# Optimization experiments

Hardware: AMD Instinct MI355X
Metric: run time of the kernel (lower is better)

## Reference

```python
import jax, jax.numpy as jnp
import numpy as np

N = 100000      # num_nodes
E = 1600000     # num_edges
IN_DIM = 6
EDGE_DIM = 2
H = 5           # heads
C = 5           # out_channels per head (hidden_dim)
D = H * C       # 25, hidden width
L = 3           # num_layers
INV_SQRT_C = np.float32(1.0 / np.sqrt(C))


def setup_inputs() -> dict:
    key = jax.random.key(0)
    ks = jax.random.split(key, 18)
    s = 0.1
    inp = {
        "x": jax.random.normal(ks[0], (N, IN_DIM), dtype=jnp.float32),
        "edge_index": jax.random.randint(ks[1], (2, E), 0, N, dtype=jnp.int64),
        "edge_attr": jax.random.normal(ks[2], (E, EDGE_DIM), dtype=jnp.float32),
        # input projection
        "Wi": jax.random.normal(ks[3], (IN_DIM, D), dtype=jnp.float32) * s,
        "bi": jnp.zeros((D,), dtype=jnp.float32),
        # per-layer TransformerConv params, stacked over layers
        "Wq": jax.random.normal(ks[4], (L, D, D), dtype=jnp.float32) * s,
        "bq": jnp.zeros((L, D), dtype=jnp.float32),
        "Wk": jax.random.normal(ks[5], (L, D, D), dtype=jnp.float32) * s,
        "bk": jnp.zeros((L, D), dtype=jnp.float32),
        "Wv": jax.random.normal(ks[6], (L, D, D), dtype=jnp.float32) * s,
        "bv": jnp.zeros((L, D), dtype=jnp.float32),
        "We": jax.random.normal(ks[7], (L, EDGE_DIM, D), dtype=jnp.float32) * s,  # lin_edge, no bias
        "Wskip": jax.random.normal(ks[8], (L, D, D), dtype=jnp.float32) * s,
        "bskip": jnp.zeros((L, D), dtype=jnp.float32),
        # output head
        "Wo": jax.random.normal(ks[9], (D, 1), dtype=jnp.float32) * s,
        "bo": jnp.zeros((1,), dtype=jnp.float32),
    }
    return inp


def _forward(x, edge_index, edge_attr, Wi, bi, Wq, bq, Wk, bk, Wv, bv, We, Wskip, bskip, Wo, bo):
    src, dst = edge_index[0], edge_index[1]
    h = x @ Wi + bi  # [N, D]
    for l in range(L):
        q = (h @ Wq[l] + bq[l]).reshape(N, H, C)
        k = (h @ Wk[l] + bk[l]).reshape(N, H, C)
        v = (h @ Wv[l] + bv[l]).reshape(N, H, C)
        e = (edge_attr @ We[l]).reshape(E, H, C)  # per-edge projection
        k_j = k[src] + e                           # [E, H, C]
        alpha = jnp.einsum('ehc,ehc->eh', q[dst], k_j) * INV_SQRT_C  # [E, H]
        # scatter-softmax over destination neighborhoods (PyG softmax)
        amax = jax.ops.segment_max(alpha, dst, num_segments=N)       # [N, H]
        ex = jnp.exp(alpha - amax[dst])
        denom = jax.ops.segment_sum(ex, dst, num_segments=N)         # [N, H]
        alpha = ex / (denom[dst] + 1e-16)
        msg = (v[src] + e) * alpha[:, :, None]                       # [E, H, C]
        out = jax.ops.segment_sum(msg, dst, num_segments=N).reshape(N, D)
        h = out + h @ Wskip[l] + bskip[l]          # root_weight skip
    return jax.nn.sigmoid(h @ Wo + bo)             # [N, 1]


def reference(x, edge_index, edge_attr, Wi, bi, Wq, bq, Wk, bk, Wv, bv, We, Wskip, bskip, Wo, bo):
    return _forward(x, edge_index, edge_attr, Wi, bi, Wq, bq, Wk, bk, Wv, bv, We, Wskip, bskip, Wo, bo)
```

## Files before the change

### kernel.cpp

```cpp
#include <hip/hip_runtime.h>
#include <hip/hip_bf16.h>
#include <math.h>

#define NN 100000
#define NE 1600000
#define IN_DIM 6
#define EDGE_DIM 2
#define HH 5
#define CC 5
#define DD 25
#define DS 32
#define INV_SQRT_C 0.4472135954999579f
#define NBUK 200
#define BUKW 500
#define CAP 10000
#define KPB 800
#define CH (NE / KPB)
#define NPB 48
#define NBLK ((NN + NPB - 1) / NPB)
#define NBD ((NN + 255) / 256)


__device__ __forceinline__ unsigned int f2bf(float f) {
    unsigned int u = __float_as_uint(f);
    return (u + 0x7fffu + ((u >> 16) & 1u)) >> 16;
}
__device__ __forceinline__ float bflo(unsigned int u) { return __uint_as_float(u << 16); }
__device__ __forceinline__ float bfhi(unsigned int u) { return __uint_as_float(u & 0xffff0000u); }

__global__ __launch_bounds__(256) void k_part(const int* __restrict__ ei,
                                              const float* __restrict__ ea,
                                              int* __restrict__ cursor,
                                              uint2* __restrict__ slab) {
    __shared__ int sdst[CH];
    __shared__ int scnt[NBUK];
    __shared__ int sbase[NBUK];
    __shared__ int swp[NBUK];
    int base = blockIdx.x * CH;
    for (int i = threadIdx.x; i < NBUK; i += 256) scnt[i] = 0;
    __syncthreads();
    for (int i = threadIdx.x; i < CH; i += 256) {
        int dst = ei[NE + base + i];
        sdst[i] = dst;
        atomicAdd(&scnt[dst / BUKW], 1);
    }
    __syncthreads();
    for (int i = threadIdx.x; i < NBUK; i += 256) {
        sbase[i] = i * CAP + atomicAdd(&cursor[i], scnt[i]);
        swp[i] = 0;
    }
    __syncthreads();
    for (int i = threadIdx.x; i < CH; i += 256) {
        int dst = sdst[i];
        int b = dst / BUKW;
        int src = ei[base + i];
        float2 eav = ((const float2*)ea)[base + i];
        int p = sbase[b] + atomicAdd(&swp[b], 1);
        uint2 r;
        r.x = (unsigned)src | ((unsigned)(dst - b * BUKW) << 17);
        r.y = f2bf(eav.x) | (f2bf(eav.y) << 16);
        slab[p] = r;
    }
}

__global__ __launch_bounds__(512) void k_place(const int* __restrict__ cursor,
                                               const uint2* __restrict__ slab,
                                               int* __restrict__ rowptr,
                                               uint2* __restrict__ csr) {
    __shared__ int hist[BUKW];
    __shared__ int cur[BUKW];
    __shared__ int s[512];
    int b = blockIdx.x;
    int t = threadIdx.x;
    int node0 = b * BUKW;
    int begin = b * CAP;
    int cnt = cursor[b];
    s[t] = (t < NBUK && t < b) ? cursor[t] : 0;
    __syncthreads();
    for (int off = 256; off > 0; off >>= 1) {
        if (t < off) s[t] += s[t + off];
        __syncthreads();
    }
    int bOff = s[0];
    __syncthreads();
    for (int i = t; i < BUKW; i += 512) hist[i] = 0;
    __syncthreads();
    for (int i = t; i < cnt; i += 512) {
        uint2 r = slab[begin + i];
        atomicAdd(&hist[r.x >> 17], 1);
    }
    __syncthreads();
    int hv = (t < BUKW) ? hist[t] : 0;
    s[t] = hv;
    __syncthreads();
    for (int off = 1; off < 512; off <<= 1) {
        int u = (t >= off) ? s[t - off] : 0;
        __syncthreads();
        s[t] += u;
        __syncthreads();
    }
    if (t < BUKW) {
        int o = bOff + s[t] - hv;
        rowptr[node0 + t] = o;
        cur[t] = o;
    }
    if (b == NBUK - 1 && t == 0) rowptr[NN] = NE;
    __syncthreads();
    for (int i = t; i < cnt; i += 512) {
        uint2 r = slab[begin + i];
        int dl = (int)(r.x >> 17);
        int p = atomicAdd(&cur[dl], 1);
        uint2 o;
        o.x = r.x & 0x1FFFFu;
        o.y = r.y;
        csr[p] = o;
    }
}

__global__ void k_dh(const int* __restrict__ rowptr, int* __restrict__ bhist) {
    __shared__ int lh[256];
    int t = threadIdx.x;
    lh[t] = 0;
    __syncthreads();
    int i = blockIdx.x * 256 + t;
    if (i < NN) {
        int d = rowptr[i + 1] - rowptr[i];
        atomicAdd(&lh[d > 255 ? 255 : d], 1);
    }
    __syncthreads();
    bhist[t * NBD + blockIdx.x] = lh[t];
}

__global__ __launch_bounds__(512) void k_ds(int* __restrict__ bhist, int* __restrict__ binTot) {
    __shared__ int s[512];
    int bin = blockIdx.x;
    int t = threadIdx.x;
    int v = (t < NBD) ? bhist[bin * NBD + t] : 0;
    s[t] = v;
    __syncthreads();
    for (int off = 1; off < 512; off <<= 1) {
        int u = (t >= off) ? s[t - off] : 0;
        __syncthreads();
        s[t] += u;
        __syncthreads();
    }
    if (t < NBD) bhist[bin * NBD + t] = s[t] - v;
    if (t == 511) binTot[bin] = s[511];
}

__global__ void k_ds2(int* __restrict__ binTot, int* __restrict__ binOff) {
    __shared__ int s[256];
    int t = threadIdx.x;
    int v = binTot[t];
    s[t] = v;
    __syncthreads();
    for (int off = 1; off < 256; off <<= 1) {
        int u = (t >= off) ? s[t - off] : 0;
        __syncthreads();
        s[t] += u;
        __syncthreads();
    }
    binOff[t] = s[t] - v;
}

__global__ void k_dp(const int* __restrict__ rowptr, const int* __restrict__ bhist,
                     const int* __restrict__ binOff, int* __restrict__ perm) {
    __shared__ int lcur[256];
    int t = threadIdx.x;
    lcur[t] = 0;
    __syncthreads();
    int i = blockIdx.x * 256 + t;
    if (i < NN) {
        int d = rowptr[i + 1] - rowptr[i];
        if (d > 255) d = 255;
        int r = atomicAdd(&lcur[d], 1);
        perm[binOff[d] + bhist[d * NBD + blockIdx.x] + r] = i;
    }
}

__global__ void k_input_proj(const float* __restrict__ x, const float* __restrict__ Wi,
                             const float* __restrict__ bi, float* __restrict__ h) {
    __shared__ float sW[IN_DIM * DD];
    __shared__ float sb[DD];
    int t = threadIdx.x;
    if (t < IN_DIM * DD) sW[t] = Wi[t];
    if (t < DD) sb[t] = bi[t];
    __syncthreads();
    int tid = blockIdx.x * blockDim.x + t;
    int n = tid / DD, d = tid - n * DD;
    if (n >= NN) return;
    float acc = sb[d];
    const float* xr = x + n * IN_DIM;
#pragma unroll
    for (int i = 0; i < IN_DIM; i++) acc += xr[i] * sW[i * DD + d];
    h[n * DS + d] = acc;
}

__global__ void k_qkv_skip(const float* __restrict__ h,
                           const float* __restrict__ Wq, const float* __restrict__ bq,
                           const float* __restrict__ Wk, const float* __restrict__ bk,
                           const float* __restrict__ Wv, const float* __restrict__ bv,
                           const float* __restrict__ Ws, const float* __restrict__ bs,
                           __hip_bfloat16* __restrict__ q, __hip_bfloat16* __restrict__ kv,
                           float* __restrict__ hout) {
    __shared__ float sWq[DD * DD], sWk[DD * DD], sWv[DD * DD], sWs[DD * DD];
    __shared__ float sb[4 * DD];
    for (int i = threadIdx.x; i < DD * DD; i += blockDim.x) {
        sWq[i] = Wq[i]; sWk[i] = Wk[i]; sWv[i] = Wv[i]; sWs[i] = Ws[i];
    }
    if (threadIdx.x < DD) {
        sb[threadIdx.x]          = bq[threadIdx.x];
        sb[DD + threadIdx.x]     = bk[threadIdx.x];
        sb[2 * DD + threadIdx.x] = bv[threadIdx.x];
        sb[3 * DD + threadIdx.x] = bs[threadIdx.x];
    }
    __syncthreads();
    int tid = blockIdx.x * blockDim.x + threadIdx.x;
    int n = tid / DD, d = tid - n * DD;
    if (n >= NN) return;
    float aq = sb[d], ak = sb[DD + d], av = sb[2 * DD + d], asv = sb[3 * DD + d];
    const float* hr = h + (size_t)n * DS;
#pragma unroll
    for (int i = 0; i < DD; i++) {
        float hv = hr[i];
        aq  += hv * sWq[i * DD + d];
        ak  += hv * sWk[i * DD + d];
        av  += hv * sWv[i * DD + d];
        asv += hv * sWs[i * DD + d];
    }
    int h5 = d / 5, c5 = d - 5 * h5;
    q[(size_t)n * 40 + 8 * h5 + c5] = __float2bfloat16(aq * INV_SQRT_C);
    size_t rb = (size_t)n * 64;
    kv[rb + 8 * h5 + c5] = __float2bfloat16(ak);
    if (c5 < 3) kv[rb + 8 * h5 + 5 + c5] = __float2bfloat16(av);
    else        kv[rb + 40 + 2 * h5 + (c5 - 3)] = __float2bfloat16(av);
    hout[(size_t)n * DS + d] = asv;
}

__global__ __launch_bounds__(256) void k_edge_fused(
    const int* __restrict__ rowptr, const uint2* __restrict__ csr,
    const int* __restrict__ perm,
    const float* __restrict__ We, const __hip_bfloat16* __restrict__ q,
    const __hip_bfloat16* __restrict__ kv, float* __restrict__ hout,
    int fuse_head, const float* __restrict__ Wo, const float* __restrict__ bo,
    float* __restrict__ out) {
    __shared__ float sWe[EDGE_DIM * DD];
    __shared__ float sWo[DD];
    __shared__ float sbo;
    if (threadIdx.x < EDGE_DIM * DD) sWe[threadIdx.x] = We[threadIdx.x];
    if (threadIdx.x < DD) sWo[threadIdx.x] = Wo[threadIdx.x];
    if (threadIdx.x == 0) sbo = bo[0];
    __syncthreads();
    int lane = threadIdx.x & 63;
    int wv   = threadIdx.x >> 6;
    int grp  = lane / 5;
    int h    = lane - grp * 5;
    int idx  = blockIdx.x * NPB + wv * 12 + grp;
    bool act = (grp < 12) && (idx < NN);
    int node = 0;

    int beg = 0, end = 0;
    float qa0 = 0, qa1 = 0, qa2 = 0, qa3 = 0, qa4 = 0, qwx = 0, qwy = 0;
    if (act) {
        node = perm[idx];
        beg = rowptr[node];
        end = rowptr[node + 1];
        uint4 qc = *(const uint4*)(q + (size_t)node * 40 + 8 * h);
        qa0 = bflo(qc.x); qa1 = bfhi(qc.x); qa2 = bflo(qc.y); qa3 = bfhi(qc.y); qa4 = bflo(qc.z);
        const float* wx = &sWe[5 * h];
        const float* wy = &sWe[DD + 5 * h];
        qwx = qa0 * wx[0] + qa1 * wx[1] + qa2 * wx[2] + qa3 * wx[3] + qa4 * wx[4];
        qwy = qa0 * wy[0] + qa1 * wy[1] + qa2 * wy[2] + qa3 * wy[3] + qa4 * wy[4];
    }

    float l = 0.f, Sx = 0.f, Sy = 0.f;
    float a0 = 0.f, a1 = 0.f, a2 = 0.f, a3 = 0.f, a4 = 0.f;

    int p = beg;
    for (; p + 2 <= end; p += 2) {
        uint2 r0 = csr[p];
        uint2 r1 = csr[p + 1];
        const __hip_bfloat16* b0 = kv + ((size_t)r0.x << 6);
        const __hip_bfloat16* b1 = kv + ((size_t)r1.x << 6);
        uint4 A0 = *(const uint4*)(b0 + 8 * h);
        unsigned int B0 = *(const unsigned int*)(b0 + 40 + 2 * h);
        uint4 A1 = *(const uint4*)(b1 + 8 * h);
        unsigned int B1 = *(const unsigned int*)(b1 + 40 + 2 * h);
        {
            float eax = bflo(r0.y), eay = bfhi(r0.y);
            float k0 = bflo(A0.x), k1 = bfhi(A0.x), k2 = bflo(A0.y), k3 = bfhi(A0.y), k4 = bflo(A0.z);
            float v0 = bfhi(A0.z), v1 = bflo(A0.w), v2 = bfhi(A0.w), v3 = bflo(B0), v4 = bfhi(B0);
            float s = qa0 * k0 + qa1 * k1 + qa2 * k2 + qa3 * k3 + qa4 * k4 + eax * qwx + eay * qwy;
            float cf = __expf(s);
            l += cf; Sx += cf * eax; Sy += cf * eay;
            a0 += cf * v0; a1 += cf * v1; a2 += cf * v2; a3 += cf * v3; a4 += cf * v4;
        }
        {
            float eax = bflo(r1.y), eay = bfhi(r1.y);
            float k0 = bflo(A1.x), k1 = bfhi(A1.x), k2 = bflo(A1.y), k3 = bfhi(A1.y), k4 = bflo(A1.z);
            float v0 = bfhi(A1.z), v1 = bflo(A1.w), v2 = bfhi(A1.w), v3 = bflo(B1), v4 = bfhi(B1);
            float s = qa0 * k0 + qa1 * k1 + qa2 * k2 + qa3 * k3 + qa4 * k4 + eax * qwx + eay * qwy;
            float cf = __expf(s);
            l += cf; Sx += cf * eax; Sy += cf * eay;
            a0 += cf * v0; a1 += cf * v1; a2 += cf * v2; a3 += cf * v3; a4 += cf * v4;
        }
    }
    if (p < end) {
        uint2 r0 = csr[p];
        const __hip_bfloat16* b0 = kv + ((size_t)r0.x << 6);
        uint4 A0 = *(const uint4*)(b0 + 8 * h);
        unsigned int B0 = *(const unsigned int*)(b0 + 40 + 2 * h);
        float eax = bflo(r0.y), eay = bfhi(r0.y);
        float k0 = bflo(A0.x), k1 = bfhi(A0.x), k2 = bflo(A0.y), k3 = bfhi(A0.y), k4 = bflo(A0.z);
        float v0 = bfhi(A0.z), v1 = bflo(A0.w), v2 = bfhi(A0.w), v3 = bflo(B0), v4 = bfhi(B0);
        float s = qa0 * k0 + qa1 * k1 + qa2 * k2 + qa3 * k3 + qa4 * k4 + eax * qwx + eay * qwy;
        float cf = __expf(s);
        l += cf; Sx += cf * eax; Sy += cf * eay;
        a0 += cf * v0; a1 += cf * v1; a2 += cf * v2; a3 += cf * v3; a4 += cf * v4;
    }

    float dot = 0.f;
    if (act) {
        float inv = 1.0f / (l + 1e-16f);
        const float* wx = &sWe[5 * h];
        const float* wy = &sWe[DD + 5 * h];
        float* ho = hout + (size_t)node * DS + 5 * h;
        float n0 = ho[0] + (a0 + Sx * wx[0] + Sy * wy[0]) * inv;
        float n1 = ho[1] + (a1 + Sx * wx[1] + Sy * wy[1]) * inv;
        float n2 = ho[2] + (a2 + Sx * wx[2] + Sy * wy[2]) * inv;
        float n3 = ho[3] + (a3 + Sx * wx[3] + Sy * wy[3]) * inv;
        float n4 = ho[4] + (a4 + Sx * wx[4] + Sy * wy[4]) * inv;
        ho[0] = n0; ho[1] = n1; ho[2] = n2; ho[3] = n3; ho[4] = n4;
        if (fuse_head) {
            const float* wo = &sWo[5 * h];
            dot = n0 * wo[0] + n1 * wo[1] + n2 * wo[2] + n3 * wo[3] + n4 * wo[4];
        }
    }
    if (fuse_head) {
        float dsum = dot;
#pragma unroll
        for (int k = 1; k < 5; k++) dsum += __shfl(dot, (grp * 5 + k) & 63, 64);
        if (act && h == 0) out[node] = 1.0f / (1.0f + __expf(-(dsum + sbo)));
    }
}

extern "C" void kernel_launch(void* const* d_in, const int* in_sizes, int n_in,
                              void* d_out, int out_size, void* d_ws, size_t ws_size,
                              hipStream_t stream) {
    const float* x     = (const float*)d_in[0];
    const int*   ei    = (const int*)d_in[1];
    const float* ea    = (const float*)d_in[2];
    const float* Wi    = (const float*)d_in[3];
    const float* bi    = (const float*)d_in[4];
    const float* Wq    = (const float*)d_in[5];
    const float* bq    = (const float*)d_in[6];
    const float* Wk    = (const float*)d_in[7];
    const float* bk    = (const float*)d_in[8];
    const float* Wv    = (const float*)d_in[9];
    const float* bv    = (const float*)d_in[10];
    const float* We    = (const float*)d_in[11];
    const float* Wskip = (const float*)d_in[12];
    const float* bskip = (const float*)d_in[13];
    const float* Wo    = (const float*)d_in[14];
    const float* bo    = (const float*)d_in[15];
    float* out = (float*)d_out;
    (void)in_sizes; (void)n_in; (void)out_size; (void)ws_size;

    char* wsb = (char*)d_ws;
    size_t off = 0;
    auto alloc = [&](size_t bytes) {
        void* p = wsb + off;
        off += (bytes + 127) & ~(size_t)127;
        return p;
    };
    uint2* slab   = (uint2*)alloc((size_t)NBUK * CAP * sizeof(uint2));
    uint2* csr    = (uint2*)alloc((size_t)NE * sizeof(uint2));
    __hip_bfloat16* kvrec = (__hip_bfloat16*)alloc((size_t)NN * 64 * 2);
    __hip_bfloat16* qrec  = (__hip_bfloat16*)alloc((size_t)NN * 40 * 2);
    float* hA     = (float*)alloc((size_t)NN * DS * sizeof(float));
    float* hB     = (float*)alloc((size_t)NN * DS * sizeof(float));
    int*   rowptr = (int*)alloc((size_t)(NN + 1) * sizeof(int));
    int*   cursor = (int*)alloc((size_t)NBUK * sizeof(int));
    int*   bhist  = (int*)alloc((size_t)256 * NBD * sizeof(int));
    int*   binTot = (int*)alloc(256 * sizeof(int));
    int*   binOff = (int*)alloc(256 * sizeof(int));
    int*   perm   = (int*)alloc((size_t)NN * sizeof(int));

    dim3 blk(256);
    int gND = (NN * DD + 255) / 256;

    hipMemsetAsync(cursor, 0, (size_t)NBUK * sizeof(int), stream);
    k_part<<<KPB, blk, 0, stream>>>(ei, ea, cursor, slab);
    k_place<<<NBUK, dim3(512), 0, stream>>>(cursor, slab, rowptr, csr);
    k_dh<<<NBD, blk, 0, stream>>>(rowptr, bhist);
    k_ds<<<256, dim3(512), 0, stream>>>(bhist, binTot);
    k_ds2<<<1, blk, 0, stream>>>(binTot, binOff);
    k_dp<<<NBD, blk, 0, stream>>>(rowptr, bhist, binOff, perm);

    k_input_proj<<<gND, blk, 0, stream>>>(x, Wi, bi, hA);

    float* hc = hA;
    float* hn = hB;
    for (int l = 0; l < 3; l++) {
        k_qkv_skip<<<gND, blk, 0, stream>>>(hc,
                                            Wq + (size_t)l * DD * DD, bq + (size_t)l * DD,
                                            Wk + (size_t)l * DD * DD, bk + (size_t)l * DD,
                                            Wv + (size_t)l * DD * DD, bv + (size_t)l * DD,
                                            Wskip + (size_t)l * DD * DD, bskip + (size_t)l * DD,
                                            qrec, kvrec, hn);
        k_edge_fused<<<NBLK, blk, 0, stream>>>(rowptr, csr, perm,
                                               We + (size_t)l * EDGE_DIM * DD,
                                               qrec, kvrec, hn,
                                               (l == 2) ? 1 : 0, Wo, bo, out);
        float* t = hc; hc = hn; hn = t;
    }
}
```

Baseline: 375.6 us.

## Unroll edge loop by four, pad bucket cursors, reverse degree-sorted node order

The edge aggregation loop is unrolled from two to four edges per iteration, issuing all gathers before any math, to raise memory-level parallelism. The global bucket cursors are spaced 16 ints apart so atomics from different blocks hit separate cache lines instead of contending on shared ones. The degree-sorted permutation is reversed so high-degree nodes are scheduled first, which should reduce tail imbalance. More live registers from the wider unroll could reduce occupancy.

```diff
diff --git a/kernel.cpp b/kernel.cpp
--- a/kernel.cpp
+++ b/kernel.cpp
@@ -19,6 +19,7 @@
 #define NPB 48
 #define NBLK ((NN + NPB - 1) / NPB)
 #define NBD ((NN + 255) / 256)
+#define CSTR 16
 
 
 __device__ __forceinline__ unsigned int f2bf(float f) {
@@ -46,7 +47,7 @@
     }
     __syncthreads();
     for (int i = threadIdx.x; i < NBUK; i += 256) {
-        sbase[i] = i * CAP + atomicAdd(&cursor[i], scnt[i]);
+        sbase[i] = i * CAP + atomicAdd(&cursor[i * CSTR], scnt[i]);
         swp[i] = 0;
     }
     __syncthreads();
@@ -74,8 +75,8 @@
     int t = threadIdx.x;
     int node0 = b * BUKW;
     int begin = b * CAP;
-    int cnt = cursor[b];
-    s[t] = (t < NBUK && t < b) ? cursor[t] : 0;
+    int cnt = cursor[b * CSTR];
+    s[t] = (t < NBUK && t < b) ? cursor[t * CSTR] : 0;
     __syncthreads();
     for (int off = 256; off > 0; off >>= 1) {
         if (t < off) s[t] += s[t + off];
@@ -174,7 +175,8 @@
         int d = rowptr[i + 1] - rowptr[i];
         if (d > 255) d = 255;
         int r = atomicAdd(&lcur[d], 1);
-        perm[binOff[d] + bhist[d * NBD + blockIdx.x] + r] = i;
+        int pos = binOff[d] + bhist[d * NBD + blockIdx.x] + r;
+        perm[NN - 1 - pos] = i;
     }
 }
 
@@ -235,6 +237,20 @@
     if (c5 < 3) kv[rb + 8 * h5 + 5 + c5] = __float2bfloat16(av);
     else        kv[rb + 40 + 2 * h5 + (c5 - 3)] = __float2bfloat16(av);
     hout[(size_t)n * DS + d] = asv;
+}
+
+struct EState { float l, Sx, Sy, a0, a1, a2, a3, a4; };
+
+__device__ __forceinline__ void edge_acc(EState& st, uint2 rec, uint4 A, unsigned int B,
+                                         float qa0, float qa1, float qa2, float qa3, float qa4,
+                                         float qwx, float qwy) {
+    float eax = bflo(rec.y), eay = bfhi(rec.y);
+    float k0 = bflo(A.x), k1 = bfhi(A.x), k2 = bflo(A.y), k3 = bfhi(A.y), k4 = bflo(A.z);
+    float v0 = bfhi(A.z), v1 = bflo(A.w), v2 = bfhi(A.w), v3 = bflo(B), v4 = bfhi(B);
+    float s = qa0 * k0 + qa1 * k1 + qa2 * k2 + qa3 * k3 + qa4 * k4 + eax * qwx + eay * qwy;
+    float cf = __expf(s);
+    st.l += cf; st.Sx += cf * eax; st.Sy += cf * eay;
+    st.a0 += cf * v0; st.a1 += cf * v1; st.a2 += cf * v2; st.a3 += cf * v3; st.a4 += cf * v4;
 }
 
 __global__ __launch_bounds__(256) void k_edge_fused(
@@ -273,63 +289,47 @@
         qwy = qa0 * wy[0] + qa1 * wy[1] + qa2 * wy[2] + qa3 * wy[3] + qa4 * wy[4];
     }
 
-    float l = 0.f, Sx = 0.f, Sy = 0.f;
-    float a0 = 0.f, a1 = 0.f, a2 = 0.f, a3 = 0.f, a4 = 0.f;
+    EState st = {0.f, 0.f, 0.f, 0.f, 0.f, 0.f, 0.f, 0.f};
 
     int p = beg;
-    for (; p + 2 <= end; p += 2) {
-        uint2 r0 = csr[p];
-        uint2 r1 = csr[p + 1];
+    for (; p + 4 <= end; p += 4) {
+        uint2 r0 = csr[p], r1 = csr[p + 1], r2 = csr[p + 2], r3 = csr[p + 3];
         const __hip_bfloat16* b0 = kv + ((size_t)r0.x << 6);
         const __hip_bfloat16* b1 = kv + ((size_t)r1.x << 6);
+        const __hip_bfloat16* b2 = kv + ((size_t)r2.x << 6);
+        const __hip_bfloat16* b3 = kv + ((size_t)r3.x << 6);
         uint4 A0 = *(const uint4*)(b0 + 8 * h);
+        uint4 A1 = *(const uint4*)(b1 + 8 * h);
+        uint4 A2 = *(const uint4*)(b2 + 8 * h);
+        uint4 A3 = *(const uint4*)(b3 + 8 * h);
         unsigned int B0 = *(const unsigned int*)(b0 + 40 + 2 * h);
-        uint4 A1 = *(const uint4*)(b1 + 8 * h);
         unsigned int B1 = *(const unsigned int*)(b1 + 40 + 2 * h);
-        {
-            float eax = bflo(r0.y), eay = bfhi(r0.y);
-            float k0 = bflo(A0.x), k1 = bfhi(A0.x), k2 = bflo(A0.y), k3 = bfhi(A0.y), k4 = bflo(A0.z);
-            float v0 = bfhi(A0.z), v1 = bflo(A0.w), v2 = bfhi(A0.w), v3 = bflo(B0), v4 = bfhi(B0);
-            float s = qa0 * k0 + qa1 * k1 + qa2 * k2 + qa3 * k3 + qa4 * k4 + eax * qwx + eay * qwy;
-            float cf = __expf(s);
-            l += cf; Sx += cf * eax; Sy += cf * eay;
-            a0 += cf * v0; a1 += cf * v1; a2 += cf * v2; a3 += cf * v3; a4 += cf * v4;
-        }
-        {
-            float eax = bflo(r1.y), eay = bfhi(r1.y);
-            float k0 = bflo(A1.x), k1 = bfhi(A1.x), k2 = bflo(A1.y), k3 = bfhi(A1.y), k4 = bflo(A1.z);
-            float v0 = bfhi(A1.z), v1 = bflo(A1.w), v2 = bfhi(A1.w), v3 = bflo(B1), v4 = bfhi(B1);
-            float s = qa0 * k0 + qa1 * k1 + qa2 * k2 + qa3 * k3 + qa4 * k4 + eax * qwx + eay * qwy;
-            float cf = __expf(s);
-            l += cf; Sx += cf * eax; Sy += cf * eay;
-            a0 += cf * v0; a1 += cf * v1; a2 += cf * v2; a3 += cf * v3; a4 += cf * v4;
-        }
-    }
-    if (p < end) {
+        unsigned int B2 = *(const unsigned int*)(b2 + 40 + 2 * h);
+        unsigned int B3 = *(const unsigned int*)(b3 + 40 + 2 * h);
+        edge_acc(st, r0, A0, B0, qa0, qa1, qa2, qa3, qa4, qwx, qwy);
+        edge_acc(st, r1, A1, B1, qa0, qa1, qa2, qa3, qa4, qwx, qwy);
+        edge_acc(st, r2, A2, B2, qa0, qa1, qa2, qa3, qa4, qwx, qwy);
+        edge_acc(st, r3, A3, B3, qa0, qa1, qa2, qa3, qa4, qwx, qwy);
+    }
+    for (; p < end; ++p) {
         uint2 r0 = csr[p];
         const __hip_bfloat16* b0 = kv + ((size_t)r0.x << 6);
         uint4 A0 = *(const uint4*)(b0 + 8 * h);
         unsigned int B0 = *(const unsigned int*)(b0 + 40 + 2 * h);
-        float eax = bflo(r0.y), eay = bfhi(r0.y);
-        float k0 = bflo(A0.x), k1 = bfhi(A0.x), k2 = bflo(A0.y), k3 = bfhi(A0.y), k4 = bflo(A0.z);
-        float v0 = bfhi(A0.z), v1 = bflo(A0.w), v2 = bfhi(A0.w), v3 = bflo(B0), v4 = bfhi(B0);
-        float s = qa0 * k0 + qa1 * k1 + qa2 * k2 + qa3 * k3 + qa4 * k4 + eax * qwx + eay * qwy;
-        float cf = __expf(s);
-        l += cf; Sx += cf * eax; Sy += cf * eay;
-        a0 += cf * v0; a1 += cf * v1; a2 += cf * v2; a3 += cf * v3; a4 += cf * v4;
+        edge_acc(st, r0, A0, B0, qa0, qa1, qa2, qa3, qa4, qwx, qwy);
     }
 
     float dot = 0.f;
     if (act) {
-        float inv = 1.0f / (l + 1e-16f);
+        float inv = 1.0f / (st.l + 1e-16f);
         const float* wx = &sWe[5 * h];
         const float* wy = &sWe[DD + 5 * h];
         float* ho = hout + (size_t)node * DS + 5 * h;
-        float n0 = ho[0] + (a0 + Sx * wx[0] + Sy * wy[0]) * inv;
-        float n1 = ho[1] + (a1 + Sx * wx[1] + Sy * wy[1]) * inv;
-        float n2 = ho[2] + (a2 + Sx * wx[2] + Sy * wy[2]) * inv;
-        float n3 = ho[3] + (a3 + Sx * wx[3] + Sy * wy[3]) * inv;
-        float n4 = ho[4] + (a4 + Sx * wx[4] + Sy * wy[4]) * inv;
+        float n0 = ho[0] + (st.a0 + st.Sx * wx[0] + st.Sy * wy[0]) * inv;
+        float n1 = ho[1] + (st.a1 + st.Sx * wx[1] + st.Sy * wy[1]) * inv;
+        float n2 = ho[2] + (st.a2 + st.Sx * wx[2] + st.Sy * wy[2]) * inv;
+        float n3 = ho[3] + (st.a3 + st.Sx * wx[3] + st.Sy * wy[3]) * inv;
+        float n4 = ho[4] + (st.a4 + st.Sx * wx[4] + st.Sy * wy[4]) * inv;
         ho[0] = n0; ho[1] = n1; ho[2] = n2; ho[3] = n3; ho[4] = n4;
         if (fuse_head) {
             const float* wo = &sWo[5 * h];
@@ -380,7 +380,7 @@
     float* hA     = (float*)alloc((size_t)NN * DS * sizeof(float));
     float* hB     = (float*)alloc((size_t)NN * DS * sizeof(float));
     int*   rowptr = (int*)alloc((size_t)(NN + 1) * sizeof(int));
-    int*   cursor = (int*)alloc((size_t)NBUK * sizeof(int));
+    int*   cursor = (int*)alloc((size_t)NBUK * CSTR * sizeof(int));
     int*   bhist  = (int*)alloc((size_t)256 * NBD * sizeof(int));
     int*   binTot = (int*)alloc(256 * sizeof(int));
     int*   binOff = (int*)alloc(256 * sizeof(int));
@@ -389,7 +389,7 @@
     dim3 blk(256);
     int gND = (NN * DD + 255) / 256;
 
-    hipMemsetAsync(cursor, 0, (size_t)NBUK * sizeof(int), stream);
+    (void)hipMemsetAsync(cursor, 0, (size_t)NBUK * CSTR * sizeof(int), stream);
     k_part<<<KPB, blk, 0, stream>>>(ei, ea, cursor, slab);
     k_place<<<NBUK, dim3(512), 0, stream>>>(cursor, slab, rowptr, csr);
     k_dh<<<NBD, blk, 0, stream>>>(rowptr, bhist);
```

Result: faster. 360.4 us (-4.0%).
